# Kernel optimization log

Measured on AMD Instinct MI355X. Metric: run time of the kernel, lower is better.

The kernel has to match this reference:

```python
import jax, jax.numpy as jnp
import numpy as np

N_HEADS = 8
D_HEAD = 64
SCALE = D_HEAD ** -0.5


def setup_inputs() -> dict:
    key = jax.random.key(0)
    k1, k2, k3 = jax.random.split(key, 3)
    B, H, W, C = 16, 32, 32, 512
    ft = jax.random.normal(k1, (B, H, W, C), dtype=jnp.float32)
    # Dense layers: to_qkv -> n_heads*n_dim_heads*3 = 1536 units, to_out -> n_channels
    w_qkv = jax.random.normal(k2, (C, N_HEADS * D_HEAD * 3), dtype=jnp.float32) * (C ** -0.5)
    b_qkv = jnp.zeros((N_HEADS * D_HEAD * 3,), dtype=jnp.float32)
    w_out = jax.random.normal(k3, (N_HEADS * D_HEAD, C), dtype=jnp.float32) * ((N_HEADS * D_HEAD) ** -0.5)
    b_out = jnp.zeros((C,), dtype=jnp.float32)
    return {"ft": ft, "w_qkv": w_qkv, "b_qkv": b_qkv, "w_out": w_out, "b_out": b_out}


def reference(ft, w_qkv, b_qkv, w_out, b_out):
    B, H, W, C = ft.shape
    N = H * W
    x = ft.reshape(B, N, C)                       # b (h w) c
    qkv = x @ w_qkv + b_qkv                       # b n (heads * 3*d_head)
    qkv = qkv.reshape(B, N, N_HEADS, 3 * D_HEAD)  # 'b x (h d) -> b x h d'
    q, k, v = jnp.split(qkv, 3, axis=-1)          # each: b n heads d_head
    attn = jnp.einsum('bxhd,byhd->bxyh', q, k) * SCALE
    attn = jax.nn.softmax(attn, axis=2)           # softmax over key axis y
    res = jnp.einsum('bxyh,byhd->bxhd', attn, v)  # b x h d
    res = res.reshape(B, N, N_HEADS * D_HEAD)     # 'b x h d -> b x (h d)'
    res = res @ w_out + b_out
    res = res + x                                 # residual with pre-qkv flattened input
    return res.reshape(B, H, W, C)
```

## Files before the change

### kernel.cpp

```cpp
#include <hip/hip_runtime.h>
#include <hip/hip_bf16.h>

using u16 = unsigned short;
using u32 = unsigned int;
typedef __attribute__((ext_vector_type(8))) short short8;
typedef __attribute__((ext_vector_type(4))) float f32x4;

#define MFMA16(A, B, C) __builtin_amdgcn_mfma_f32_16x16x32_bf16((A), (B), (C), 0, 0, 0)

__device__ __forceinline__ u16 f2bf(float f) {
  union { float f; u32 i; } v; v.f = f;
  u32 x = v.i;
  return (u16)((x + 0x7fffu + ((x >> 16) & 1u)) >> 16);
}
__device__ __forceinline__ u32 pkbf(float a, float b) {
  union { __hip_bfloat162 h; u32 u; } v;
  v.h = __float22bfloat162_rn(make_float2(a, b));
  return v.u;
}
__device__ __forceinline__ void gl16(const u16* g, u16* l) {
  __builtin_amdgcn_global_load_lds(
      (const __attribute__((address_space(1))) u32*)g,
      (__attribute__((address_space(3))) u32*)l, 16, 0, 0);
}

__global__ __launch_bounds__(256) void conv_x(const float* __restrict__ X,
                                              u16* __restrict__ Xbf) {
  const int i = (blockIdx.x * 256 + threadIdx.x) * 8;
  float4 a = *(const float4*)(X + i);
  float4 b = *(const float4*)(X + i + 4);
  uint4 o;
  o.x = pkbf(a.x, a.y); o.y = pkbf(a.z, a.w);
  o.z = pkbf(b.x, b.y); o.w = pkbf(b.z, b.w);
  *(uint4*)(Xbf + i) = o;
}

__global__ __launch_bounds__(256) void transpose_w(
    const float* __restrict__ Wq, const float* __restrict__ Wo,
    u16* __restrict__ Wqt, u16* __restrict__ Wot) {
  const int z = blockIdx.z;
  if (z == 1 && blockIdx.x >= 16) return;
  const float* src = z ? Wo : Wq;
  u16* dst = z ? Wot : Wqt;
  const int ncols = z ? 512 : 1536;
  __shared__ float tile[32][33];
  const int t = threadIdx.x;
  const int kt = blockIdx.y * 32, nt = blockIdx.x * 32;
  const int r = t >> 3, c4 = (t & 7) * 4;
  float4 v = *(const float4*)(src + (size_t)(kt + r) * ncols + nt + c4);
  tile[r][c4 + 0] = v.x; tile[r][c4 + 1] = v.y;
  tile[r][c4 + 2] = v.z; tile[r][c4 + 3] = v.w;
  __syncthreads();
  uint2 p = make_uint2(pkbf(tile[c4 + 0][r], tile[c4 + 1][r]),
                       pkbf(tile[c4 + 2][r], tile[c4 + 3][r]));
  *(uint2*)(dst + (size_t)(nt + r) * 512 + kt + c4) = p;
}

__global__ __launch_bounds__(256) void qkv_gemm(
    const u16* __restrict__ Xbf, const u16* __restrict__ Wt,
    const float* __restrict__ Bias,
    u16* __restrict__ Qp, u16* __restrict__ Kp, u16* __restrict__ Vt) {
  __shared__ u16 Xs[128][32];
  __shared__ u16 Ws[128][32];
  const int t = threadIdx.x;
  const int bm = blockIdx.y * 128, bn = blockIdx.x * 128;
  const int w = t >> 6, lane = t & 63, quad = lane >> 4, l16 = lane & 15;
  const int mtb = (w >> 1) * 64, ntb = (w & 1) * 64;
  const int rr = lane >> 2;
  const int gch = ((lane & 3) ^ ((lane >> 3) & 3)) * 8;
  const int sw = (quad ^ ((l16 >> 1) & 3)) * 8;

  const u16* xg0 = Xbf + (size_t)(bm + w * 16 + rr) * 512 + gch;
  const u16* xg1 = xg0 + (size_t)64 * 512;
  const u16* wg0 = Wt + (size_t)(bn + w * 16 + rr) * 512 + gch;
  const u16* wg1 = wg0 + (size_t)64 * 512;
  u16* xl0 = &Xs[w * 16][0]; u16* xl1 = &Xs[64 + w * 16][0];
  u16* wl0 = &Ws[w * 16][0]; u16* wl1 = &Ws[64 + w * 16][0];

  f32x4 acc[4][4];
  const f32x4 z4 = {0.f, 0.f, 0.f, 0.f};
  #pragma unroll
  for (int mi = 0; mi < 4; mi++)
    #pragma unroll
    for (int ni = 0; ni < 4; ni++) acc[mi][ni] = z4;

  for (int k0 = 0; k0 < 512; k0 += 32) {
    gl16(xg0 + k0, xl0);
    gl16(xg1 + k0, xl1);
    gl16(wg0 + k0, wl0);
    gl16(wg1 + k0, wl1);
    __syncthreads();
    short8 af[4], bf4[4];
    #pragma unroll
    for (int mi = 0; mi < 4; mi++)
      af[mi] = *(const short8*)&Xs[mtb + mi * 16 + l16][sw];
    #pragma unroll
    for (int ni = 0; ni < 4; ni++)
      bf4[ni] = *(const short8*)&Ws[ntb + ni * 16 + l16][sw];
    #pragma unroll
    for (int mi = 0; mi < 4; mi++)
      #pragma unroll
      for (int ni = 0; ni < 4; ni++)
        acc[mi][ni] = MFMA16(af[mi], bf4[ni], acc[mi][ni]);
    __syncthreads();
  }

  #pragma unroll
  for (int ni = 0; ni < 4; ni++) {
    const int g = bn + ntb + ni * 16;
    const int h = g / 192, rm = g % 192;
    const int type = rm >> 6, dbase = rm & 63;
    const float bias = Bias[g + l16];
    const float qsc = (type == 0) ? 0.125f * 1.44269504088896340736f : 1.0f;
    #pragma unroll
    for (int mi = 0; mi < 4; mi++) {
      const int row0 = bm + mtb + mi * 16 + quad * 4;
      const int b = row0 >> 10, n0 = row0 & 1023;
      const size_t bh = (size_t)(b * 8 + h) * 65536;
      if (type == 2) {
        uint2 p = make_uint2(pkbf(acc[mi][ni][0] + bias, acc[mi][ni][1] + bias),
                             pkbf(acc[mi][ni][2] + bias, acc[mi][ni][3] + bias));
        *(uint2*)(Vt + bh + (size_t)(dbase + l16) * 1024 + n0) = p;
      } else {
        u16* dst = (type ? Kp : Qp) + bh;
        #pragma unroll
        for (int r = 0; r < 4; r++)
          dst[(size_t)(n0 + r) * 64 + dbase + l16] =
              f2bf((acc[mi][ni][r] + bias) * qsc);
      }
    }
  }
}

__global__ __launch_bounds__(512, 4) void attn_mfma(
    const u16* __restrict__ Qp, const u16* __restrict__ Kp,
    const u16* __restrict__ Vt, u16* __restrict__ ATT) {
  __shared__ u16 Ks[128][72];
  __shared__ u16 Vs[64][136];
  const int t = threadIdx.x, w = t >> 6, lane = t & 63;
  const int quad = lane >> 4, l16 = lane & 15;
  const int bx = blockIdx.x;
  const int c = bx & 7, g = bx >> 3;
  const int qt = g & 7, u = g >> 3;
  const int bh_id = u * 8 + c;
  const int b = bh_id >> 3, h = bh_id & 7;
  const size_t bh = (size_t)bh_id * 65536;
  const u16* Qb = Qp + bh;
  const u16* Kb = Kp + bh;
  const u16* Vb = Vt + bh;
  const int q0 = qt * 128 + w * 16;

  const int kkey = t >> 2, koff = (t & 3) * 16;
  const int vrow = t >> 3, voff = (t & 7) * 16;
  const u16* Kg = Kb + (size_t)kkey * 64 + koff;
  const u16* Vg = Vb + (size_t)vrow * 1024 + voff;

  short8 qf[2];
  #pragma unroll
  for (int ks = 0; ks < 2; ks++)
    qf[ks] = *(const short8*)(Qb + (size_t)(q0 + l16) * 64 + ks * 32 + quad * 8);

  float l_ = 0.f;
  f32x4 Of[4];
  const f32x4 z4 = {0.f, 0.f, 0.f, 0.f};
  #pragma unroll
  for (int ni = 0; ni < 4; ni++) Of[ni] = z4;

  uint4 kr0 = *(const uint4*)(Kg);
  uint4 kr1 = *(const uint4*)(Kg + 8);
  uint4 vr0 = *(const uint4*)(Vg);
  uint4 vr1 = *(const uint4*)(Vg + 8);

  for (int kt = 0; kt < 8; kt++) {
    __syncthreads();
    *(uint4*)&Ks[kkey][koff]     = kr0;
    *(uint4*)&Ks[kkey][koff + 8] = kr1;
    *(uint4*)&Vs[vrow][voff]     = vr0;
    *(uint4*)&Vs[vrow][voff + 8] = vr1;
    if (kt < 7) {
      kr0 = *(const uint4*)(Kg + (kt + 1) * 8192);
      kr1 = *(const uint4*)(Kg + (kt + 1) * 8192 + 8);
      vr0 = *(const uint4*)(Vg + (kt + 1) * 128);
      vr1 = *(const uint4*)(Vg + (kt + 1) * 128 + 8);
    }
    __syncthreads();

    f32x4 s[8];
    #pragma unroll
    for (int nt = 0; nt < 8; nt++) s[nt] = z4;
    #pragma unroll
    for (int nt = 0; nt < 8; nt++) {
      short8 k0f = *(const short8*)&Ks[nt * 16 + l16][quad * 8];
      short8 k1f = *(const short8*)&Ks[nt * 16 + l16][quad * 8 + 32];
      s[nt] = MFMA16(k0f, qf[0], s[nt]);
      s[nt] = MFMA16(k1f, qf[1], s[nt]);
    }
    u32 e[8], o[8];
    #pragma unroll
    for (int nt = 0; nt < 8; nt++) {
      float p0 = __builtin_amdgcn_exp2f(s[nt][0]);
      float p1 = __builtin_amdgcn_exp2f(s[nt][1]);
      float p2 = __builtin_amdgcn_exp2f(s[nt][2]);
      float p3 = __builtin_amdgcn_exp2f(s[nt][3]);
      l_ += (p0 + p1) + (p2 + p3);
      const u32 lo = pkbf(p0, p1), hi = pkbf(p2, p3);
      if (nt & 1) { o[(nt >> 1) * 2] = lo; o[(nt >> 1) * 2 + 1] = hi; }
      else        { e[(nt >> 1) * 2] = lo; e[(nt >> 1) * 2 + 1] = hi; }
    }
    #pragma unroll
    for (int i = 0; i < 8; i++) {
      auto t01 = __builtin_amdgcn_permlane32_swap(e[i], o[i], false, false);
      auto xy  = __builtin_amdgcn_permlane16_swap(t01[0], t01[1], false, false);
      e[i] = xy[0]; o[i] = xy[1];
    }
    #pragma unroll
    for (int ks = 0; ks < 4; ks++) {
      union { short8 v; u32 u[4]; } pa;
      pa.u[0] = e[2 * ks]; pa.u[1] = e[2 * ks + 1];
      pa.u[2] = o[2 * ks]; pa.u[3] = o[2 * ks + 1];
      #pragma unroll
      for (int ni = 0; ni < 4; ni++) {
        short8 vf = *(const short8*)&Vs[ni * 16 + l16][ks * 32 + quad * 8];
        Of[ni] = MFMA16(pa.v, vf, Of[ni]);
      }
    }
  }
  l_ += __shfl_xor(l_, 16);
  l_ += __shfl_xor(l_, 32);
  float lv[4];
  #pragma unroll
  for (int r = 0; r < 4; r++) lv[r] = __shfl(l_, quad * 4 + r);
  #pragma unroll
  for (int r = 0; r < 4; r++) {
    const float inv = 1.0f / lv[r];
    const int row = b * 1024 + q0 + quad * 4 + r;
    #pragma unroll
    for (int ni = 0; ni < 4; ni++)
      ATT[(size_t)row * 512 + h * 64 + ni * 16 + l16] = f2bf(Of[ni][r] * inv);
  }
}

__global__ __launch_bounds__(256) void out_proj(
    const u16* __restrict__ A, const u16* __restrict__ Wt,
    const float* __restrict__ Bias, const float* __restrict__ FT,
    float* __restrict__ OUT) {
  __shared__ u16 As[128][32];
  __shared__ u16 Ws[128][32];
  const int t = threadIdx.x;
  const int bm = blockIdx.y * 128, bn = blockIdx.x * 128;
  const int w = t >> 6, lane = t & 63, quad = lane >> 4, l16 = lane & 15;
  const int mtb = (w >> 1) * 64, ntb = (w & 1) * 64;
  const int rr = lane >> 2;
  const int gch = ((lane & 3) ^ ((lane >> 3) & 3)) * 8;
  const int sw = (quad ^ ((l16 >> 1) & 3)) * 8;

  const u16* ag0 = A + (size_t)(bm + w * 16 + rr) * 512 + gch;
  const u16* ag1 = ag0 + (size_t)64 * 512;
  const u16* wg0 = Wt + (size_t)(bn + w * 16 + rr) * 512 + gch;
  const u16* wg1 = wg0 + (size_t)64 * 512;
  u16* al0 = &As[w * 16][0]; u16* al1 = &As[64 + w * 16][0];
  u16* wl0 = &Ws[w * 16][0]; u16* wl1 = &Ws[64 + w * 16][0];

  f32x4 acc[4][4];
  const f32x4 z4 = {0.f, 0.f, 0.f, 0.f};
  #pragma unroll
  for (int mi = 0; mi < 4; mi++)
    #pragma unroll
    for (int ni = 0; ni < 4; ni++) acc[mi][ni] = z4;

  for (int k0 = 0; k0 < 512; k0 += 32) {
    gl16(ag0 + k0, al0);
    gl16(ag1 + k0, al1);
    gl16(wg0 + k0, wl0);
    gl16(wg1 + k0, wl1);
    __syncthreads();
    short8 af[4], bf4[4];
    #pragma unroll
    for (int mi = 0; mi < 4; mi++)
      af[mi] = *(const short8*)&As[mtb + mi * 16 + l16][sw];
    #pragma unroll
    for (int ni = 0; ni < 4; ni++)
      bf4[ni] = *(const short8*)&Ws[ntb + ni * 16 + l16][sw];
    #pragma unroll
    for (int mi = 0; mi < 4; mi++)
      #pragma unroll
      for (int ni = 0; ni < 4; ni++)
        acc[mi][ni] = MFMA16(af[mi], bf4[ni], acc[mi][ni]);
    __syncthreads();
  }

  #pragma unroll
  for (int ni = 0; ni < 4; ni++) {
    const int g = bn + ntb + ni * 16;
    const float bias = Bias[g + l16];
    #pragma unroll
    for (int mi = 0; mi < 4; mi++) {
      const int row0 = bm + mtb + mi * 16 + quad * 4;
      #pragma unroll
      for (int r = 0; r < 4; r++) {
        const size_t idx = (size_t)(row0 + r) * 512 + g + l16;
        OUT[idx] = acc[mi][ni][r] + bias + FT[idx];
      }
    }
  }
}

extern "C" void kernel_launch(void* const* d_in, const int* in_sizes, int n_in,
                              void* d_out, int out_size, void* d_ws, size_t ws_size,
                              hipStream_t stream) {
  const float* ft    = (const float*)d_in[0];
  const float* w_qkv = (const float*)d_in[1];
  const float* b_qkv = (const float*)d_in[2];
  const float* w_out = (const float*)d_in[3];
  const float* b_out = (const float*)d_in[4];
  float* out = (float*)d_out;

  char* p = (char*)d_ws;
  u16* Xbf    = (u16*)(p);
  u16* ATT    = Xbf;
  u16* Wqkv_t = (u16*)(p + 16777216);
  u16* Wout_t = (u16*)(p + 18350080);
  u16* Qp     = (u16*)(p + 18874368);
  u16* Kp     = (u16*)(p + 35651584);
  u16* Vt     = (u16*)(p + 52428800);

  conv_x     <<<4096, 256, 0, stream>>>(ft, Xbf);
  transpose_w<<<dim3(48, 16, 2), 256, 0, stream>>>(w_qkv, w_out, Wqkv_t, Wout_t);
  qkv_gemm   <<<dim3(12, 128), 256, 0, stream>>>(Xbf, Wqkv_t, b_qkv, Qp, Kp, Vt);
  attn_mfma  <<<dim3(1024), 512, 0, stream>>>(Qp, Kp, Vt, ATT);
  out_proj   <<<dim3(4, 128), 256, 0, stream>>>(ATT, Wout_t, b_out, ft, out);
}
```

Measured before the change: 206.6 us.

## Load K/V tiles directly to LDS with XOR-swizzled layout

Replaces the register-staged K/V prefetch with global_load_lds direct-to-LDS copies. Padding is removed from the shared tiles in favour of an XOR swizzle that avoids bank conflicts on the MFMA fragment reads. The QK^T and exp loops are fused so fewer score registers are live, and launch bounds rise to 6 waves per SIMD. The register-based double buffering is lost, so global load latency is no longer overlapped with compute in the same block; higher occupancy is meant to hide it instead.

```diff
diff --git a/kernel.cpp b/kernel.cpp
--- a/kernel.cpp
+++ b/kernel.cpp
@@ -132,11 +132,11 @@
   }
 }
 
-__global__ __launch_bounds__(512, 4) void attn_mfma(
+__global__ __launch_bounds__(512, 6) void attn_mfma(
     const u16* __restrict__ Qp, const u16* __restrict__ Kp,
     const u16* __restrict__ Vt, u16* __restrict__ ATT) {
-  __shared__ u16 Ks[128][72];
-  __shared__ u16 Vs[64][136];
+  __shared__ u16 Ks[128][64];
+  __shared__ u16 Vs[64][128];
   const int t = threadIdx.x, w = t >> 6, lane = t & 63;
   const int quad = lane >> 4, l16 = lane & 15;
   const int bx = blockIdx.x;
@@ -150,10 +150,22 @@
   const u16* Vb = Vt + bh;
   const int q0 = qt * 128 + w * 16;
 
-  const int kkey = t >> 2, koff = (t & 3) * 16;
-  const int vrow = t >> 3, voff = (t & 7) * 16;
-  const u16* Kg = Kb + (size_t)kkey * 64 + koff;
-  const u16* Vg = Vb + (size_t)vrow * 1024 + voff;
+  const u16* kgA = Kb + (size_t)(t >> 3) * 64 + ((t & 7) ^ ((t >> 3) & 7)) * 8;
+  const u16* kgB = kgA + (size_t)64 * 64;
+  const u16* vgA = Vb + (size_t)(t >> 4) * 1024 + ((t & 15) ^ ((t >> 4) & 7)) * 8;
+  const u16* vgB = vgA + (size_t)32 * 1024;
+  u16* ksl0 = &Ks[0][0] + w * 512;  u16* ksl1 = ksl0 + 4096;
+  u16* vsl0 = &Vs[0][0] + w * 512;  u16* vsl1 = vsl0 + 4096;
+
+  const int m7 = l16 & 7;
+  const char* ksb = (const char*)&Ks[0][0];
+  const char* vsb = (const char*)&Vs[0][0];
+  const int kb0 = l16 * 128 + (quad ^ m7) * 16;
+  const int kb1 = kb0 ^ 64;
+  int vo[4];
+  #pragma unroll
+  for (int ks = 0; ks < 4; ks++)
+    vo[ks] = l16 * 256 + ((4 * ks + quad) ^ m7) * 16;
 
   short8 qf[2];
   #pragma unroll
@@ -166,42 +178,26 @@
   #pragma unroll
   for (int ni = 0; ni < 4; ni++) Of[ni] = z4;
 
-  uint4 kr0 = *(const uint4*)(Kg);
-  uint4 kr1 = *(const uint4*)(Kg + 8);
-  uint4 vr0 = *(const uint4*)(Vg);
-  uint4 vr1 = *(const uint4*)(Vg + 8);
-
   for (int kt = 0; kt < 8; kt++) {
     __syncthreads();
-    *(uint4*)&Ks[kkey][koff]     = kr0;
-    *(uint4*)&Ks[kkey][koff + 8] = kr1;
-    *(uint4*)&Vs[vrow][voff]     = vr0;
-    *(uint4*)&Vs[vrow][voff + 8] = vr1;
-    if (kt < 7) {
-      kr0 = *(const uint4*)(Kg + (kt + 1) * 8192);
-      kr1 = *(const uint4*)(Kg + (kt + 1) * 8192 + 8);
-      vr0 = *(const uint4*)(Vg + (kt + 1) * 128);
-      vr1 = *(const uint4*)(Vg + (kt + 1) * 128 + 8);
-    }
-    __syncthreads();
-
-    f32x4 s[8];
-    #pragma unroll
-    for (int nt = 0; nt < 8; nt++) s[nt] = z4;
+    gl16(kgA + kt * 8192, ksl0);
+    gl16(kgB + kt * 8192, ksl1);
+    gl16(vgA + kt * 128,  vsl0);
+    gl16(vgB + kt * 128,  vsl1);
+    __syncthreads();
+
+    u32 e[8], o[8];
     #pragma unroll
     for (int nt = 0; nt < 8; nt++) {
-      short8 k0f = *(const short8*)&Ks[nt * 16 + l16][quad * 8];
-      short8 k1f = *(const short8*)&Ks[nt * 16 + l16][quad * 8 + 32];
-      s[nt] = MFMA16(k0f, qf[0], s[nt]);
-      s[nt] = MFMA16(k1f, qf[1], s[nt]);
-    }
-    u32 e[8], o[8];
-    #pragma unroll
-    for (int nt = 0; nt < 8; nt++) {
-      float p0 = __builtin_amdgcn_exp2f(s[nt][0]);
-      float p1 = __builtin_amdgcn_exp2f(s[nt][1]);
-      float p2 = __builtin_amdgcn_exp2f(s[nt][2]);
-      float p3 = __builtin_amdgcn_exp2f(s[nt][3]);
+      short8 k0f = *(const short8*)(ksb + kb0 + nt * 2048);
+      short8 k1f = *(const short8*)(ksb + kb1 + nt * 2048);
+      f32x4 s = z4;
+      s = MFMA16(k0f, qf[0], s);
+      s = MFMA16(k1f, qf[1], s);
+      float p0 = __builtin_amdgcn_exp2f(s[0]);
+      float p1 = __builtin_amdgcn_exp2f(s[1]);
+      float p2 = __builtin_amdgcn_exp2f(s[2]);
+      float p3 = __builtin_amdgcn_exp2f(s[3]);
       l_ += (p0 + p1) + (p2 + p3);
       const u32 lo = pkbf(p0, p1), hi = pkbf(p2, p3);
       if (nt & 1) { o[(nt >> 1) * 2] = lo; o[(nt >> 1) * 2 + 1] = hi; }
@@ -220,7 +216,7 @@
       pa.u[2] = o[2 * ks]; pa.u[3] = o[2 * ks + 1];
       #pragma unroll
       for (int ni = 0; ni < 4; ni++) {
-        short8 vf = *(const short8*)&Vs[ni * 16 + l16][ks * 32 + quad * 8];
+        short8 vf = *(const short8*)(vsb + vo[ks] + ni * 4096);
         Of[ni] = MFMA16(pa.v, vf, Of[ni]);
       }
     }
```

Result: no change. 205.5 us (-0.6%).
